# Kernel tuning notes

Measured on AMD Instinct MI355X. Metric: run time of the kernel, lower is better.

## Reference

```python
import jax, jax.numpy as jnp
import numpy as np

N = 50000   # nodes
E = 600000  # edges (avg degree 12)
D = 128     # embedding dim (hardcoded in original: np.zeros(128))
P = 5       # propagation iterations (self.p)


def setup_inputs() -> dict:
    key = jax.random.key(0)
    ks = jax.random.split(key, 10)
    x = jax.random.normal(ks[0], (N, D), jnp.float32)
    g = jax.random.normal(ks[1], (D,), jnp.float32)
    dist = jax.random.uniform(ks[2], (E,), jnp.float32)
    w1 = jax.random.normal(ks[3], (1,), jnp.float32)
    w2 = jax.random.normal(ks[4], (1,), jnp.float32)
    w3 = jax.random.normal(ks[5], (1,), jnp.float32)
    w4 = jax.random.normal(ks[6], (1,), jnp.float32)
    w5 = jax.random.normal(ks[7], (1,), jnp.float32)
    src = jax.random.randint(ks[8], (E,), 0, N)
    dst = jax.random.randint(ks[9], (E,), 0, N)
    return {"x": x, "g": g, "dist": dist, "w1": w1, "w2": w2, "w3": w3,
            "w4": w4, "w5": w5, "src": src, "dst": dst}


def reference(x, g, dist, w1, w2, w3, w4, w5, src, dst):
    # travel_times[i] = sum_{j in N(i)} w5 * dist(i,j)  -- iteration-invariant
    travel = jax.ops.segment_sum(w5[0] * dist, src, num_segments=N)  # [N]
    # per-node affine part, constant across the P iterations
    base = w1[0] * x + w2[0] * g[None, :] + w4[0] * jax.nn.relu(travel)[:, None]  # [N, D]
    u = x  # new_u_vect starts as a copy of x
    for _ in range(P):
        # u_sum[i] = sum_{j in N(i)} u[j]  (gather + segment-sum, synchronous update)
        u_sum = jax.ops.segment_sum(u[dst], src, num_segments=N)  # [N, D]
        u = base + w3[0] * u_sum
    return jax.nn.relu(u)
```

## Files before the change

### kernel.cpp

```cpp
#include <hip/hip_runtime.h>

#define D 128
#define D4 32
#define CAP 64

typedef float v4f __attribute__((ext_vector_type(4)));
typedef _Float16 h4 __attribute__((ext_vector_type(4)));

static inline size_t align_up(size_t v, size_t a) { return (v + a - 1) & ~(a - 1); }

__global__ void fill_ell_kernel(const int* __restrict__ src,
                                const int* __restrict__ dst,
                                const float* __restrict__ dist,
                                unsigned long long* __restrict__ packed,
                                unsigned short* __restrict__ adj, int E) {
  int e = blockIdx.x * blockDim.x + threadIdx.x;
  if (e < E) {
    int s = src[e];
    unsigned long long fx = (unsigned long long)(dist[e] * 4294967296.0f);
    unsigned long long val = (1ull << 48) | fx;
    unsigned long long old = atomicAdd(&packed[s], val);
    unsigned int slot = (unsigned int)(old >> 48);
    if (slot < CAP) adj[(size_t)s * CAP + slot] = (unsigned short)dst[e];
  }
}

__global__ void pad_ell_kernel(const unsigned long long* __restrict__ packed,
                               unsigned short* __restrict__ adj, int n) {
  int i = blockIdx.x * blockDim.x + threadIdx.x;
  if (i >= n) return;
  int deg = (int)(packed[i] >> 48);
  if (deg > CAP) deg = CAP;
  int cnt = (deg + 7) & ~7;
  if (cnt > CAP) cnt = CAP;
  unsigned short zn = (unsigned short)n;
  for (int k = deg; k < cnt; ++k) adj[(size_t)i * CAP + k] = zn;
}

__global__ void base_seed_kernel(const v4f* __restrict__ x4, const v4f* __restrict__ g4,
                                 const unsigned long long* __restrict__ packed,
                                 const float* __restrict__ w1p, const float* __restrict__ w2p,
                                 const float* __restrict__ w4p, const float* __restrict__ w5p,
                                 h4* __restrict__ base, h4* __restrict__ uA,
                                 h4* __restrict__ uB, int n) {
  int i = blockIdx.x * blockDim.x + threadIdx.x;
  int node = i >> 5;
  int lane = i & 31;
  if (node > n) return;
  size_t idx = (size_t)node * 32 + lane;
  if (node == n) {
    h4 z = {0, 0, 0, 0};
    uA[idx] = z;
    uB[idx] = z;
    return;
  }
  v4f xv = x4[(size_t)node * D4 + lane];
  v4f gv = g4[lane];
  float ds = (float)(packed[node] & 0xFFFFFFFFFFFFull) * (1.0f / 4294967296.0f);
  float t = w5p[0] * ds;
  t = t > 0.f ? t : 0.f;
  v4f b = w1p[0] * xv + w2p[0] * gv;
  b += t * w4p[0];
  base[idx] = __builtin_convertvector(b, h4);
  uA[idx] = __builtin_convertvector(xv, h4);
}

__global__ __launch_bounds__(256) void prop_kernel(
    const h4* __restrict__ uin, const h4* __restrict__ base,
    const unsigned long long* __restrict__ packed,
    const unsigned short* __restrict__ adj,
    const float* __restrict__ w3p,
    void* __restrict__ uout, int n, int final_relu)
{
  int gtid = blockIdx.x * blockDim.x + threadIdx.x;
  int node = gtid >> 5;
  int lane = gtid & 31;
  if (node >= n) return;

  unsigned long long p = packed[node];
  int deg = (int)(p >> 48);
  if (deg > CAP) deg = CAP;
  int cnt = (deg + 7) & ~7;
  if (cnt > CAP) cnt = CAP;

  const unsigned short* row = adj + (size_t)node * CAP;
  int a0 = row[lane];
  int a1 = row[lane + 32];

  v4f acc0 = {0.f,0.f,0.f,0.f}, acc1 = acc0, acc2 = acc0, acc3 = acc0;

  if (cnt > 0) {
    h4 c[8];
    #pragma unroll
    for (int t = 0; t < 8; ++t) {
      int j = __shfl(a0, t, 32);
      c[t] = uin[(size_t)j * 32 + lane];
    }
    for (int k = 8; k < cnt; k += 8) {
      h4 nx[8];
      int sel = (k >= 32) ? a1 : a0;
      #pragma unroll
      for (int t = 0; t < 8; ++t) {
        int j = __shfl(sel, (k + t) & 31, 32);
        nx[t] = uin[(size_t)j * 32 + lane];
      }
      acc0 += __builtin_convertvector(c[0], v4f) + __builtin_convertvector(c[1], v4f);
      acc1 += __builtin_convertvector(c[2], v4f) + __builtin_convertvector(c[3], v4f);
      acc2 += __builtin_convertvector(c[4], v4f) + __builtin_convertvector(c[5], v4f);
      acc3 += __builtin_convertvector(c[6], v4f) + __builtin_convertvector(c[7], v4f);
      #pragma unroll
      for (int t = 0; t < 8; ++t) c[t] = nx[t];
    }
    acc0 += __builtin_convertvector(c[0], v4f) + __builtin_convertvector(c[1], v4f);
    acc1 += __builtin_convertvector(c[2], v4f) + __builtin_convertvector(c[3], v4f);
    acc2 += __builtin_convertvector(c[4], v4f) + __builtin_convertvector(c[5], v4f);
    acc3 += __builtin_convertvector(c[6], v4f) + __builtin_convertvector(c[7], v4f);
  }
  v4f asum = (acc0 + acc1) + (acc2 + acc3);

  v4f bb = __builtin_convertvector(base[(size_t)node * 32 + lane], v4f);
  v4f r = bb + w3p[0] * asum;

  if (final_relu) {
    r.x = r.x > 0.f ? r.x : 0.f;
    r.y = r.y > 0.f ? r.y : 0.f;
    r.z = r.z > 0.f ? r.z : 0.f;
    r.w = r.w > 0.f ? r.w : 0.f;
    __builtin_nontemporal_store(r, (v4f*)uout + (size_t)node * D4 + lane);
  } else {
    ((h4*)uout)[(size_t)node * 32 + lane] = __builtin_convertvector(r, h4);
  }
}

extern "C" void kernel_launch(void* const* d_in, const int* in_sizes, int n_in,
                              void* d_out, int out_size, void* d_ws, size_t ws_size,
                              hipStream_t stream) {
  const float* x    = (const float*)d_in[0];
  const float* g    = (const float*)d_in[1];
  const float* dist = (const float*)d_in[2];
  const float* w1   = (const float*)d_in[3];
  const float* w2   = (const float*)d_in[4];
  const float* w3   = (const float*)d_in[5];
  const float* w4   = (const float*)d_in[6];
  const float* w5   = (const float*)d_in[7];
  const int*   src  = (const int*)d_in[8];
  const int*   dst  = (const int*)d_in[9];

  const int N = in_sizes[0] / D;
  const int E = in_sizes[2];

  char* ws = (char*)d_ws;
  size_t o = 0;
  unsigned long long* packed = (unsigned long long*)(ws + o); o += align_up((size_t)N * 8, 256);
  unsigned short*     adj    = (unsigned short*)(ws + o);     o += align_up((size_t)N * CAP * 2, 256);
  h4*                 baseB  = (h4*)(ws + o);                 o += align_up((size_t)(N + 1) * D * 2, 256);
  h4*                 uA     = (h4*)(ws + o);                 o += align_up((size_t)(N + 1) * D * 2, 256);
  h4*                 uB     = (h4*)(ws + o);                 o += align_up((size_t)(N + 1) * D * 2, 256);
  float*              out    = (float*)d_out;

  hipMemsetAsync(packed, 0, (size_t)N * 8, stream);

  const int tb = 256;
  const int eblocks = (E + tb - 1) / tb;
  const int nblocks = (N + tb - 1) / tb;
  const int sthreads = (N + 1) * 32;
  const int sblocks = (sthreads + tb - 1) / tb;

  fill_ell_kernel<<<eblocks, tb, 0, stream>>>(src, dst, dist, packed, adj, E);
  pad_ell_kernel<<<nblocks, tb, 0, stream>>>(packed, adj, N);
  base_seed_kernel<<<sblocks, tb, 0, stream>>>((const v4f*)x, (const v4f*)g, packed,
                                               w1, w2, w4, w5, baseB, uA, uB, N);

  const int pthreads = N * 32;
  const int pblocks = (pthreads + 255) / 256;
  prop_kernel<<<pblocks, 256, 0, stream>>>(uA, baseB, packed, adj, w3, uB,  N, 0);
  prop_kernel<<<pblocks, 256, 0, stream>>>(uB, baseB, packed, adj, w3, uA,  N, 0);
  prop_kernel<<<pblocks, 256, 0, stream>>>(uA, baseB, packed, adj, w3, uB,  N, 0);
  prop_kernel<<<pblocks, 256, 0, stream>>>(uB, baseB, packed, adj, w3, uA,  N, 0);
  prop_kernel<<<pblocks, 256, 0, stream>>>(uA, baseB, packed, adj, w3, out, N, 1);
}
```

Baseline: 253.6 us.

## Split feature dim into quarters across blocks, 8 lanes per node

Each propagation block now handles 32 nodes and a single 32-feature quarter of the embedding, with 8 lanes per node. Consecutive blocks cover the four quarters of the same node chunk, so the gathered neighbor rows are reused across them. Adjacency is read as 16-byte vectors and broadcast with width-8 shuffles. The register-prefetch software pipeline is dropped in favor of a simple loop over groups of 8 neighbors. Nontemporal loads are used for packed, adj and base, which may reduce cache pollution at the cost of less latency hiding per thread.

```diff
diff --git a/kernel.cpp b/kernel.cpp
--- a/kernel.cpp
+++ b/kernel.cpp
@@ -6,6 +6,8 @@
 
 typedef float v4f __attribute__((ext_vector_type(4)));
 typedef _Float16 h4 __attribute__((ext_vector_type(4)));
+typedef unsigned int u32;
+typedef unsigned int u32v4 __attribute__((ext_vector_type(4)));
 
 static inline size_t align_up(size_t v, size_t a) { return (v + a - 1) & ~(a - 1); }
 
@@ -72,53 +74,50 @@
     const float* __restrict__ w3p,
     void* __restrict__ uout, int n, int final_relu)
 {
-  int gtid = blockIdx.x * blockDim.x + threadIdx.x;
-  int node = gtid >> 5;
-  int lane = gtid & 31;
+  int q     = blockIdx.x & 3;
+  int chunk = blockIdx.x >> 2;
+  int node  = chunk * 32 + (threadIdx.x >> 3);
+  int glane = threadIdx.x & 7;
   if (node >= n) return;
 
-  unsigned long long p = packed[node];
+  unsigned long long p = __builtin_nontemporal_load(&packed[node]);
   int deg = (int)(p >> 48);
   if (deg > CAP) deg = CAP;
-  int cnt = (deg + 7) & ~7;
-  if (cnt > CAP) cnt = CAP;
+  int cnt8 = (deg + 7) >> 3;
 
-  const unsigned short* row = adj + (size_t)node * CAP;
-  int a0 = row[lane];
-  int a1 = row[lane + 32];
+  const u32v4* row16 = (const u32v4*)(adj + (size_t)node * CAP);
+  u32v4 a = __builtin_nontemporal_load(row16 + glane);
+
+  const h4* uq = uin + (size_t)q * 8 + glane;
 
   v4f acc0 = {0.f,0.f,0.f,0.f}, acc1 = acc0, acc2 = acc0, acc3 = acc0;
 
-  if (cnt > 0) {
-    h4 c[8];
-    #pragma unroll
-    for (int t = 0; t < 8; ++t) {
-      int j = __shfl(a0, t, 32);
-      c[t] = uin[(size_t)j * 32 + lane];
-    }
-    for (int k = 8; k < cnt; k += 8) {
-      h4 nx[8];
-      int sel = (k >= 32) ? a1 : a0;
-      #pragma unroll
-      for (int t = 0; t < 8; ++t) {
-        int j = __shfl(sel, (k + t) & 31, 32);
-        nx[t] = uin[(size_t)j * 32 + lane];
-      }
-      acc0 += __builtin_convertvector(c[0], v4f) + __builtin_convertvector(c[1], v4f);
-      acc1 += __builtin_convertvector(c[2], v4f) + __builtin_convertvector(c[3], v4f);
-      acc2 += __builtin_convertvector(c[4], v4f) + __builtin_convertvector(c[5], v4f);
-      acc3 += __builtin_convertvector(c[6], v4f) + __builtin_convertvector(c[7], v4f);
-      #pragma unroll
-      for (int t = 0; t < 8; ++t) c[t] = nx[t];
-    }
-    acc0 += __builtin_convertvector(c[0], v4f) + __builtin_convertvector(c[1], v4f);
-    acc1 += __builtin_convertvector(c[2], v4f) + __builtin_convertvector(c[3], v4f);
-    acc2 += __builtin_convertvector(c[4], v4f) + __builtin_convertvector(c[5], v4f);
-    acc3 += __builtin_convertvector(c[6], v4f) + __builtin_convertvector(c[7], v4f);
+  for (int m = 0; m < cnt8; ++m) {
+    u32 b0 = __shfl((int)a.x, m, 8);
+    u32 b1 = __shfl((int)a.y, m, 8);
+    u32 b2 = __shfl((int)a.z, m, 8);
+    u32 b3 = __shfl((int)a.w, m, 8);
+    int j0 = b0 & 0xFFFF, j1 = b0 >> 16;
+    int j2 = b1 & 0xFFFF, j3 = b1 >> 16;
+    int j4 = b2 & 0xFFFF, j5 = b2 >> 16;
+    int j6 = b3 & 0xFFFF, j7 = b3 >> 16;
+    h4 v0 = uq[(size_t)j0 * 32];
+    h4 v1 = uq[(size_t)j1 * 32];
+    h4 v2 = uq[(size_t)j2 * 32];
+    h4 v3 = uq[(size_t)j3 * 32];
+    h4 v4 = uq[(size_t)j4 * 32];
+    h4 v5 = uq[(size_t)j5 * 32];
+    h4 v6 = uq[(size_t)j6 * 32];
+    h4 v7 = uq[(size_t)j7 * 32];
+    acc0 += __builtin_convertvector(v0, v4f) + __builtin_convertvector(v1, v4f);
+    acc1 += __builtin_convertvector(v2, v4f) + __builtin_convertvector(v3, v4f);
+    acc2 += __builtin_convertvector(v4, v4f) + __builtin_convertvector(v5, v4f);
+    acc3 += __builtin_convertvector(v6, v4f) + __builtin_convertvector(v7, v4f);
   }
   v4f asum = (acc0 + acc1) + (acc2 + acc3);
 
-  v4f bb = __builtin_convertvector(base[(size_t)node * 32 + lane], v4f);
+  size_t qidx = (size_t)node * 32 + q * 8 + glane;
+  v4f bb = __builtin_convertvector(__builtin_nontemporal_load(&base[qidx]), v4f);
   v4f r = bb + w3p[0] * asum;
 
   if (final_relu) {
@@ -126,9 +125,9 @@
     r.y = r.y > 0.f ? r.y : 0.f;
     r.z = r.z > 0.f ? r.z : 0.f;
     r.w = r.w > 0.f ? r.w : 0.f;
-    __builtin_nontemporal_store(r, (v4f*)uout + (size_t)node * D4 + lane);
+    __builtin_nontemporal_store(r, (v4f*)uout + qidx);
   } else {
-    ((h4*)uout)[(size_t)node * 32 + lane] = __builtin_convertvector(r, h4);
+    ((h4*)uout)[qidx] = __builtin_convertvector(r, h4);
   }
 }
 
@@ -171,8 +170,8 @@
   base_seed_kernel<<<sblocks, tb, 0, stream>>>((const v4f*)x, (const v4f*)g, packed,
                                                w1, w2, w4, w5, baseB, uA, uB, N);
 
-  const int pthreads = N * 32;
-  const int pblocks = (pthreads + 255) / 256;
+  const int chunks = (N + 31) / 32;
+  const int pblocks = chunks * 4;
   prop_kernel<<<pblocks, 256, 0, stream>>>(uA, baseB, packed, adj, w3, uB,  N, 0);
   prop_kernel<<<pblocks, 256, 0, stream>>>(uB, baseB, packed, adj, w3, uA,  N, 0);
   prop_kernel<<<pblocks, 256, 0, stream>>>(uA, baseB, packed, adj, w3, uB,  N, 0);
```

Result: slower. 321.8 us (+26.9%).

## Interleave degree and adjacency per node, drop pad kernel, mask tail indices

Applied to the files above, without the earlier changes.

Packs each node's degree/distance word and its 64 adjacency slots into one 192-byte row, so the count and the neighbour list are read from the same place. The pad kernel goes away: tail neighbours are masked in-register to the zero node, and the software-pipelined gather loop is replaced by a simpler unrolled loop. The whole row region is now memset instead of just the counters, which adds memset traffic, and the loss of prefetch overlap may cost latency hiding.

```diff
diff --git a/kernel.cpp b/kernel.cpp
--- a/kernel.cpp
+++ b/kernel.cpp
@@ -3,42 +3,43 @@
 #define D 128
 #define D4 32
 #define CAP 64
+#define RSTRIDE 192
 
 typedef float v4f __attribute__((ext_vector_type(4)));
 typedef _Float16 h4 __attribute__((ext_vector_type(4)));
 
 static inline size_t align_up(size_t v, size_t a) { return (v + a - 1) & ~(a - 1); }
 
+__device__ __forceinline__ unsigned long long* rowPacked(char* rows, int n) {
+  return (unsigned long long*)(rows + (size_t)n * RSTRIDE);
+}
+__device__ __forceinline__ const unsigned long long* rowPackedC(const char* rows, int n) {
+  return (const unsigned long long*)(rows + (size_t)n * RSTRIDE);
+}
+__device__ __forceinline__ unsigned short* rowAdj(char* rows, int n) {
+  return (unsigned short*)(rows + (size_t)n * RSTRIDE + 16);
+}
+__device__ __forceinline__ const unsigned short* rowAdjC(const char* rows, int n) {
+  return (const unsigned short*)(rows + (size_t)n * RSTRIDE + 16);
+}
+
 __global__ void fill_ell_kernel(const int* __restrict__ src,
                                 const int* __restrict__ dst,
                                 const float* __restrict__ dist,
-                                unsigned long long* __restrict__ packed,
-                                unsigned short* __restrict__ adj, int E) {
+                                char* __restrict__ rows, int E) {
   int e = blockIdx.x * blockDim.x + threadIdx.x;
   if (e < E) {
     int s = src[e];
     unsigned long long fx = (unsigned long long)(dist[e] * 4294967296.0f);
     unsigned long long val = (1ull << 48) | fx;
-    unsigned long long old = atomicAdd(&packed[s], val);
+    unsigned long long old = atomicAdd(rowPacked(rows, s), val);
     unsigned int slot = (unsigned int)(old >> 48);
-    if (slot < CAP) adj[(size_t)s * CAP + slot] = (unsigned short)dst[e];
+    if (slot < CAP) rowAdj(rows, s)[slot] = (unsigned short)dst[e];
   }
 }
 
-__global__ void pad_ell_kernel(const unsigned long long* __restrict__ packed,
-                               unsigned short* __restrict__ adj, int n) {
-  int i = blockIdx.x * blockDim.x + threadIdx.x;
-  if (i >= n) return;
-  int deg = (int)(packed[i] >> 48);
-  if (deg > CAP) deg = CAP;
-  int cnt = (deg + 7) & ~7;
-  if (cnt > CAP) cnt = CAP;
-  unsigned short zn = (unsigned short)n;
-  for (int k = deg; k < cnt; ++k) adj[(size_t)i * CAP + k] = zn;
-}
-
 __global__ void base_seed_kernel(const v4f* __restrict__ x4, const v4f* __restrict__ g4,
-                                 const unsigned long long* __restrict__ packed,
+                                 const char* __restrict__ rows,
                                  const float* __restrict__ w1p, const float* __restrict__ w2p,
                                  const float* __restrict__ w4p, const float* __restrict__ w5p,
                                  h4* __restrict__ base, h4* __restrict__ uA,
@@ -56,7 +57,8 @@
   }
   v4f xv = x4[(size_t)node * D4 + lane];
   v4f gv = g4[lane];
-  float ds = (float)(packed[node] & 0xFFFFFFFFFFFFull) * (1.0f / 4294967296.0f);
+  unsigned long long p = *rowPackedC(rows, node);
+  float ds = (float)(p & 0xFFFFFFFFFFFFull) * (1.0f / 4294967296.0f);
   float t = w5p[0] * ds;
   t = t > 0.f ? t : 0.f;
   v4f b = w1p[0] * xv + w2p[0] * gv;
@@ -67,8 +69,7 @@
 
 __global__ __launch_bounds__(256) void prop_kernel(
     const h4* __restrict__ uin, const h4* __restrict__ base,
-    const unsigned long long* __restrict__ packed,
-    const unsigned short* __restrict__ adj,
+    const char* __restrict__ rows,
     const float* __restrict__ w3p,
     void* __restrict__ uout, int n, int final_relu)
 {
@@ -77,48 +78,43 @@
   int lane = gtid & 31;
   if (node >= n) return;
 
-  unsigned long long p = packed[node];
+  unsigned long long p = *rowPackedC(rows, node);
   int deg = (int)(p >> 48);
   if (deg > CAP) deg = CAP;
-  int cnt = (deg + 7) & ~7;
-  if (cnt > CAP) cnt = CAP;
 
-  const unsigned short* row = adj + (size_t)node * CAP;
+  const unsigned short* row = rowAdjC(rows, node);
   int a0 = row[lane];
   int a1 = row[lane + 32];
 
   v4f acc0 = {0.f,0.f,0.f,0.f}, acc1 = acc0, acc2 = acc0, acc3 = acc0;
 
-  if (cnt > 0) {
-    h4 c[8];
-    #pragma unroll
-    for (int t = 0; t < 8; ++t) {
-      int j = __shfl(a0, t, 32);
-      c[t] = uin[(size_t)j * 32 + lane];
-    }
-    for (int k = 8; k < cnt; k += 8) {
-      h4 nx[8];
-      int sel = (k >= 32) ? a1 : a0;
-      #pragma unroll
-      for (int t = 0; t < 8; ++t) {
-        int j = __shfl(sel, (k + t) & 31, 32);
-        nx[t] = uin[(size_t)j * 32 + lane];
-      }
-      acc0 += __builtin_convertvector(c[0], v4f) + __builtin_convertvector(c[1], v4f);
-      acc1 += __builtin_convertvector(c[2], v4f) + __builtin_convertvector(c[3], v4f);
-      acc2 += __builtin_convertvector(c[4], v4f) + __builtin_convertvector(c[5], v4f);
-      acc3 += __builtin_convertvector(c[6], v4f) + __builtin_convertvector(c[7], v4f);
-      #pragma unroll
-      for (int t = 0; t < 8; ++t) c[t] = nx[t];
-    }
-    acc0 += __builtin_convertvector(c[0], v4f) + __builtin_convertvector(c[1], v4f);
-    acc1 += __builtin_convertvector(c[2], v4f) + __builtin_convertvector(c[3], v4f);
-    acc2 += __builtin_convertvector(c[4], v4f) + __builtin_convertvector(c[5], v4f);
-    acc3 += __builtin_convertvector(c[6], v4f) + __builtin_convertvector(c[7], v4f);
+  for (int k = 0; k < deg; k += 8) {
+    int sel = (k >= 32) ? a1 : a0;
+    int j0 = __shfl(sel, (k + 0) & 31, 32); j0 = (k + 0 < deg) ? j0 : n;
+    int j1 = __shfl(sel, (k + 1) & 31, 32); j1 = (k + 1 < deg) ? j1 : n;
+    int j2 = __shfl(sel, (k + 2) & 31, 32); j2 = (k + 2 < deg) ? j2 : n;
+    int j3 = __shfl(sel, (k + 3) & 31, 32); j3 = (k + 3 < deg) ? j3 : n;
+    int j4 = __shfl(sel, (k + 4) & 31, 32); j4 = (k + 4 < deg) ? j4 : n;
+    int j5 = __shfl(sel, (k + 5) & 31, 32); j5 = (k + 5 < deg) ? j5 : n;
+    int j6 = __shfl(sel, (k + 6) & 31, 32); j6 = (k + 6 < deg) ? j6 : n;
+    int j7 = __shfl(sel, (k + 7) & 31, 32); j7 = (k + 7 < deg) ? j7 : n;
+    h4 v0 = uin[(size_t)j0 * 32 + lane];
+    h4 v1 = uin[(size_t)j1 * 32 + lane];
+    h4 v2 = uin[(size_t)j2 * 32 + lane];
+    h4 v3 = uin[(size_t)j3 * 32 + lane];
+    h4 v4 = uin[(size_t)j4 * 32 + lane];
+    h4 v5 = uin[(size_t)j5 * 32 + lane];
+    h4 v6 = uin[(size_t)j6 * 32 + lane];
+    h4 v7 = uin[(size_t)j7 * 32 + lane];
+    acc0 += __builtin_convertvector(v0, v4f) + __builtin_convertvector(v1, v4f);
+    acc1 += __builtin_convertvector(v2, v4f) + __builtin_convertvector(v3, v4f);
+    acc2 += __builtin_convertvector(v4, v4f) + __builtin_convertvector(v5, v4f);
+    acc3 += __builtin_convertvector(v6, v4f) + __builtin_convertvector(v7, v4f);
   }
   v4f asum = (acc0 + acc1) + (acc2 + acc3);
 
-  v4f bb = __builtin_convertvector(base[(size_t)node * 32 + lane], v4f);
+  size_t idx = (size_t)node * 32 + lane;
+  v4f bb = __builtin_convertvector(base[idx], v4f);
   v4f r = bb + w3p[0] * asum;
 
   if (final_relu) {
@@ -126,9 +122,9 @@
     r.y = r.y > 0.f ? r.y : 0.f;
     r.z = r.z > 0.f ? r.z : 0.f;
     r.w = r.w > 0.f ? r.w : 0.f;
-    __builtin_nontemporal_store(r, (v4f*)uout + (size_t)node * D4 + lane);
+    __builtin_nontemporal_store(r, (v4f*)uout + idx);
   } else {
-    ((h4*)uout)[(size_t)node * 32 + lane] = __builtin_convertvector(r, h4);
+    ((h4*)uout)[idx] = __builtin_convertvector(r, h4);
   }
 }
 
@@ -151,31 +147,28 @@
 
   char* ws = (char*)d_ws;
   size_t o = 0;
-  unsigned long long* packed = (unsigned long long*)(ws + o); o += align_up((size_t)N * 8, 256);
-  unsigned short*     adj    = (unsigned short*)(ws + o);     o += align_up((size_t)N * CAP * 2, 256);
-  h4*                 baseB  = (h4*)(ws + o);                 o += align_up((size_t)(N + 1) * D * 2, 256);
-  h4*                 uA     = (h4*)(ws + o);                 o += align_up((size_t)(N + 1) * D * 2, 256);
-  h4*                 uB     = (h4*)(ws + o);                 o += align_up((size_t)(N + 1) * D * 2, 256);
-  float*              out    = (float*)d_out;
+  char* rows  = ws + o;                 o += align_up((size_t)N * RSTRIDE, 256);
+  h4*   baseB = (h4*)(ws + o);          o += align_up((size_t)(N + 1) * D * 2, 256);
+  h4*   uA    = (h4*)(ws + o);          o += align_up((size_t)(N + 1) * D * 2, 256);
+  h4*   uB    = (h4*)(ws + o);          o += align_up((size_t)(N + 1) * D * 2, 256);
+  float* out  = (float*)d_out;
 
-  hipMemsetAsync(packed, 0, (size_t)N * 8, stream);
+  hipMemsetAsync(rows, 0, (size_t)N * RSTRIDE, stream);
 
   const int tb = 256;
   const int eblocks = (E + tb - 1) / tb;
-  const int nblocks = (N + tb - 1) / tb;
   const int sthreads = (N + 1) * 32;
   const int sblocks = (sthreads + tb - 1) / tb;
 
-  fill_ell_kernel<<<eblocks, tb, 0, stream>>>(src, dst, dist, packed, adj, E);
-  pad_ell_kernel<<<nblocks, tb, 0, stream>>>(packed, adj, N);
-  base_seed_kernel<<<sblocks, tb, 0, stream>>>((const v4f*)x, (const v4f*)g, packed,
+  fill_ell_kernel<<<eblocks, tb, 0, stream>>>(src, dst, dist, rows, E);
+  base_seed_kernel<<<sblocks, tb, 0, stream>>>((const v4f*)x, (const v4f*)g, rows,
                                                w1, w2, w4, w5, baseB, uA, uB, N);
 
   const int pthreads = N * 32;
   const int pblocks = (pthreads + 255) / 256;
-  prop_kernel<<<pblocks, 256, 0, stream>>>(uA, baseB, packed, adj, w3, uB,  N, 0);
-  prop_kernel<<<pblocks, 256, 0, stream>>>(uB, baseB, packed, adj, w3, uA,  N, 0);
-  prop_kernel<<<pblocks, 256, 0, stream>>>(uA, baseB, packed, adj, w3, uB,  N, 0);
-  prop_kernel<<<pblocks, 256, 0, stream>>>(uB, baseB, packed, adj, w3, uA,  N, 0);
-  prop_kernel<<<pblocks, 256, 0, stream>>>(uA, baseB, packed, adj, w3, out, N, 1);
+  prop_kernel<<<pblocks, 256, 0, stream>>>(uA, baseB, rows, w3, uB,  N, 0);
+  prop_kernel<<<pblocks, 256, 0, stream>>>(uB, baseB, rows, w3, uA,  N, 0);
+  prop_kernel<<<pblocks, 256, 0, stream>>>(uA, baseB, rows, w3, uB,  N, 0);
+  prop_kernel<<<pblocks, 256, 0, stream>>>(uB, baseB, rows, w3, uA,  N, 0);
+  prop_kernel<<<pblocks, 256, 0, stream>>>(uA, baseB, rows, w3, out, N, 1);
 }
```

Result: no change. 254.5 us (+0.4%).
